# Performance work log

Measured on AMD Instinct MI355X. Metric: run time of the kernel, lower is better.

Reference implementation:

```python
import jax, jax.numpy as jnp
import numpy as np

N_NODES = 100000
D = 256          # embedding_dim
K = 5            # num_communities
B = 8192         # events in batch
R = 32           # negatives per event


def setup_inputs() -> dict:
    key = jax.random.key(0)
    ks = jax.random.split(key, 12)
    src = jax.random.randint(ks[0], (B,), 0, N_NODES)
    dst = jax.random.randint(ks[1], (B,), 0, N_NODES)
    neg = jax.random.randint(ks[2], (B, R), 0, N_NODES)
    ts = jax.random.uniform(ks[3], (B,), dtype=jnp.float32) * 100.0 + 50.0
    edge_idxs = jax.random.randint(ks[4], (B,), 0, 1000000)
    # node state table and last-update times (buffers in the torch module)
    state = jax.random.normal(ks[5], (N_NODES, D), dtype=jnp.float32)
    last_t = jax.random.uniform(ks[6], (N_NODES,), dtype=jnp.float32) * 50.0
    # decay parameter and CommunityProjector MLP params
    log_decay = jnp.asarray(0.0, dtype=jnp.float32)
    W1 = jax.random.normal(ks[7], (D, D), dtype=jnp.float32) / np.sqrt(D)
    b1 = jnp.zeros((D,), dtype=jnp.float32)
    W2 = jax.random.normal(ks[8], (D, K), dtype=jnp.float32) / np.sqrt(D)
    b2 = jnp.zeros((K,), dtype=jnp.float32)
    return {"src": src, "dst": dst, "neg": neg, "ts": ts, "edge_idxs": edge_idxs,
            "state": state, "last_t": last_t, "log_decay": log_decay,
            "W1": W1, "b1": b1, "W2": W2, "b2": b2}


def _proj_state(nodes, t, state, last_t, log_decay):
    # dt = clamp(t - last_t[nodes], 0); s_proj = state[nodes] * exp(-softplus(log_decay)*dt)
    dt = jnp.maximum(t - last_t[nodes], 0.0)
    decay = jax.nn.softplus(log_decay)
    gate = jnp.exp(-decay * dt)[..., None]
    return state[nodes] * gate


def _projector(x, W1, b1, W2, b2):
    # Linear -> ReLU -> (Dropout eval = identity) -> Linear -> Softmax
    h = jax.nn.relu(x @ W1 + b1)
    return jax.nn.softmax(h @ W2 + b2, axis=-1)


def reference(src, dst, neg, ts, edge_idxs, state, last_t, log_decay, W1, b1, W2, b2):
    s_src = _proj_state(src, ts, state, last_t, log_decay)          # [B, D]
    s_dst = _proj_state(dst, ts, state, last_t, log_decay)          # [B, D]
    s_neg = _proj_state(neg, ts[:, None], state, last_t, log_decay) # [B, R, D]
    p_src = _projector(s_src, W1, b1, W2, b2)                       # [B, K]
    p_dst = _projector(s_dst, W1, b1, W2, b2)                       # [B, K]
    p_neg = _projector(s_neg, W1, b1, W2, b2)                       # [B, R, K]
    return p_src, p_dst, p_neg
```

## Files before the change

### kernel.cpp

```cpp
#include <hip/hip_runtime.h>
#include <hip/hip_bf16.h>

#define B_EV    8192
#define R_NEG   32
#define DIM     256
#define K_COM   5
#define M_ROWS  (B_EV * (R_NEG + 2))
#define BM      64
#define NT      (M_ROWS / BM)
#define NBLK    512
#define N_NODES_C 100000

typedef _Float16 f16x8 __attribute__((ext_vector_type(8)));
typedef float    f32x4 __attribute__((ext_vector_type(4)));

__global__ __launch_bounds__(256, 2) void fused_kernel(
    const int* __restrict__ src, const int* __restrict__ dst,
    const int* __restrict__ neg, const float* __restrict__ ts,
    const float* __restrict__ state, const float* __restrict__ last_t,
    const float* __restrict__ log_decay,
    const float* __restrict__ W1, const float* __restrict__ b1,
    const float* __restrict__ W2, const float* __restrict__ b2,
    float* __restrict__ out)
{
    __shared__ f16x8 xt8[2048];
    __shared__ int   node_s[64];
    __shared__ float gate_s[64];
    __shared__ float part[4][64][K_COM];

    const int tid  = threadIdx.x;
    const int lane = tid & 63;
    const int w    = tid >> 6;
    const int l15  = lane & 15;
    const int g    = lane >> 4;

    float ld    = log_decay[0];
    float decay = (ld > 30.f) ? ld : log1pf(expf(ld));

    f16x8 bfrag[4][8];
    {
        const float* wbase = W1 + (size_t)(g * 8) * DIM + w * 64 + l15;
        #pragma unroll
        for (int nt = 0; nt < 4; ++nt)
            #pragma unroll
            for (int ks = 0; ks < 8; ++ks)
                #pragma unroll
                for (int j = 0; j < 8; ++j)
                    bfrag[nt][ks][j] = (_Float16)wbase[(size_t)(ks * 32 + j) * DIM + nt * 16];
    }

    for (int t = blockIdx.x; t < NT; t += NBLK) {
        const int m0 = t * BM;

        if (tid < 64) {
            int m  = m0 + tid;
            int be = m / 34;
            int sl = m - be * 34;
            int node = (sl == 0) ? src[be] : (sl == 1) ? dst[be] : neg[be * R_NEG + (sl - 2)];
            if ((unsigned)node >= (unsigned)N_NODES_C) node = 0;
            float dtv = fmaxf(ts[be] - last_t[node], 0.f);
            node_s[tid] = node;
            gate_s[tid] = expf(-decay * dtv);
        }
        __syncthreads();

        {
            int c8 = tid & 31;
            int rb = tid >> 5;
            #pragma unroll
            for (int it = 0; it < 8; ++it) {
                int r = it * 8 + rb;
                int node = node_s[r];
                float gg = gate_s[r];
                const float* sp = state + (size_t)node * DIM + c8 * 8;
                float4 v0 = *(const float4*)(sp);
                float4 v1 = *(const float4*)(sp + 4);
                f16x8 pk;
                pk[0] = (_Float16)(v0.x * gg); pk[1] = (_Float16)(v0.y * gg);
                pk[2] = (_Float16)(v0.z * gg); pk[3] = (_Float16)(v0.w * gg);
                pk[4] = (_Float16)(v1.x * gg); pk[5] = (_Float16)(v1.y * gg);
                pk[6] = (_Float16)(v1.z * gg); pk[7] = (_Float16)(v1.w * gg);
                xt8[(r * 32 + c8) ^ (r & 7)] = pk;
            }
        }
        __syncthreads();

        f32x4 acc[4][4];
        #pragma unroll
        for (int a = 0; a < 4; ++a)
            #pragma unroll
            for (int bb = 0; bb < 4; ++bb)
                acc[a][bb] = (f32x4){0.f, 0.f, 0.f, 0.f};

        #pragma unroll
        for (int ks = 0; ks < 8; ++ks) {
            f16x8 av[4];
            #pragma unroll
            for (int mt = 0; mt < 4; ++mt) {
                int row = mt * 16 + l15;
                av[mt] = xt8[(row * 32 + ks * 4 + g) ^ (row & 7)];
            }
            #pragma unroll
            for (int nt = 0; nt < 4; ++nt)
                #pragma unroll
                for (int mt = 0; mt < 4; ++mt)
                    acc[mt][nt] = __builtin_amdgcn_mfma_f32_16x16x32_f16(av[mt], bfrag[nt][ks], acc[mt][nt], 0, 0, 0);
        }

        float b1v[4];
        float w2v[4][K_COM];
        #pragma unroll
        for (int nt = 0; nt < 4; ++nt) {
            int col = w * 64 + nt * 16 + l15;
            b1v[nt] = b1[col];
            #pragma unroll
            for (int k = 0; k < K_COM; ++k) w2v[nt][k] = W2[col * K_COM + k];
        }

        #pragma unroll
        for (int mt = 0; mt < 4; ++mt) {
            #pragma unroll
            for (int reg = 0; reg < 4; ++reg) {
                float p[K_COM] = {0.f, 0.f, 0.f, 0.f, 0.f};
                #pragma unroll
                for (int nt = 0; nt < 4; ++nt) {
                    float h = fmaxf(acc[mt][nt][reg] + b1v[nt], 0.f);
                    #pragma unroll
                    for (int k = 0; k < K_COM; ++k) p[k] += h * w2v[nt][k];
                }
                #pragma unroll
                for (int off = 8; off >= 1; off >>= 1)
                    #pragma unroll
                    for (int k = 0; k < K_COM; ++k) p[k] += __shfl_xor(p[k], off);
                if (l15 == 0) {
                    int row = mt * 16 + g * 4 + reg;
                    #pragma unroll
                    for (int k = 0; k < K_COM; ++k) part[w][row][k] = p[k];
                }
            }
        }
        __syncthreads();

        if (tid < 64) {
            float lg[K_COM];
            #pragma unroll
            for (int k = 0; k < K_COM; ++k)
                lg[k] = part[0][tid][k] + part[1][tid][k] + part[2][tid][k] + part[3][tid][k] + b2[k];
            float mx = lg[0];
            #pragma unroll
            for (int k = 1; k < K_COM; ++k) mx = fmaxf(mx, lg[k]);
            float sum = 0.f;
            #pragma unroll
            for (int k = 0; k < K_COM; ++k) { lg[k] = expf(lg[k] - mx); sum += lg[k]; }
            float inv = 1.f / sum;

            int m  = m0 + tid;
            int be = m / 34;
            int sl = m - be * 34;
            float* op;
            if (sl == 0)      op = out + (size_t)be * K_COM;
            else if (sl == 1) op = out + (size_t)B_EV * K_COM + (size_t)be * K_COM;
            else              op = out + (size_t)2 * B_EV * K_COM + ((size_t)be * R_NEG + (sl - 2)) * K_COM;
            #pragma unroll
            for (int k = 0; k < K_COM; ++k) op[k] = lg[k] * inv;
        }
    }
}

extern "C" void kernel_launch(void* const* d_in, const int* in_sizes, int n_in,
                              void* d_out, int out_size, void* d_ws, size_t ws_size,
                              hipStream_t stream) {
    const int*   src       = (const int*)d_in[0];
    const int*   dst       = (const int*)d_in[1];
    const int*   neg       = (const int*)d_in[2];
    const float* ts        = (const float*)d_in[3];
    const float* state     = (const float*)d_in[5];
    const float* last_t    = (const float*)d_in[6];
    const float* log_decay = (const float*)d_in[7];
    const float* W1        = (const float*)d_in[8];
    const float* b1        = (const float*)d_in[9];
    const float* W2        = (const float*)d_in[10];
    const float* b2        = (const float*)d_in[11];

    fused_kernel<<<dim3(NBLK), dim3(256), 0, stream>>>(
        src, dst, neg, ts, state, last_t, log_decay, W1, b1, W2, b2,
        (float*)d_out);
}
```

Measured before the change: 326.0 us.

## Precompute state@W1 for all nodes, then gather and apply gate per row

The per-row decay gate is a scalar, so (state*gate)@W1 equals gate*(state@W1). The first kernel multiplies the whole 100k-node state table by W1 once and writes an fp16 table Y to the workspace. A second kernel gathers Y rows per event, applies the gate, bias, ReLU, the W2 projection and the softmax. This replaces a GEMM over about 278k gathered fp32 rows with a dense GEMM over 100k rows plus half-width gathers, at the cost of a 51 MB intermediate write and a second launch. The old fused kernel is kept as a fallback, with its W1 fragments unrolled into named registers, when the workspace is too small.

```diff
diff --git a/kernel.cpp b/kernel.cpp
--- a/kernel.cpp
+++ b/kernel.cpp
@@ -6,15 +6,216 @@
 #define DIM     256
 #define K_COM   5
 #define M_ROWS  (B_EV * (R_NEG + 2))
-#define BM      64
-#define NT      (M_ROWS / BM)
+#define NNODE   100000
+#define Y_BYTES ((size_t)NNODE * DIM * 2)
+#define S1_BLK  ((NNODE + 63) / 64)
+#define S2_BLK  2048
 #define NBLK    512
-#define N_NODES_C 100000
+#define NT_FB   (M_ROWS / 64)
 
 typedef _Float16 f16x8 __attribute__((ext_vector_type(8)));
 typedef float    f32x4 __attribute__((ext_vector_type(4)));
 
-__global__ __launch_bounds__(256, 2) void fused_kernel(
+#define MF(a, b, c) __builtin_amdgcn_mfma_f32_16x16x32_f16((a), (b), (c), 0, 0, 0)
+
+#define LDB2(BV, NT_, KS_) do {                                          \
+    const float* p_ = wbase + (size_t)((KS_) * 32) * DIM + (NT_) * 16;   \
+    BV[0] = (_Float16)p_[0 * DIM]; BV[1] = (_Float16)p_[1 * DIM];        \
+    BV[2] = (_Float16)p_[2 * DIM]; BV[3] = (_Float16)p_[3 * DIM];        \
+    BV[4] = (_Float16)p_[4 * DIM]; BV[5] = (_Float16)p_[5 * DIM];        \
+    BV[6] = (_Float16)p_[6 * DIM]; BV[7] = (_Float16)p_[7 * DIM];        \
+} while (0)
+
+#define KSTEP2(KS_, B0_, B1_) do {                                       \
+    f16x8 av0 = xt8[(( 0 + l15) * 32 + (KS_) * 4 + g) ^ (l15 & 7)];      \
+    f16x8 av1 = xt8[((16 + l15) * 32 + (KS_) * 4 + g) ^ (l15 & 7)];      \
+    f16x8 av2 = xt8[((32 + l15) * 32 + (KS_) * 4 + g) ^ (l15 & 7)];      \
+    f16x8 av3 = xt8[((48 + l15) * 32 + (KS_) * 4 + g) ^ (l15 & 7)];      \
+    acc[0][0] = MF(av0, B0_, acc[0][0]); acc[1][0] = MF(av1, B0_, acc[1][0]); \
+    acc[2][0] = MF(av2, B0_, acc[2][0]); acc[3][0] = MF(av3, B0_, acc[3][0]); \
+    acc[0][1] = MF(av0, B1_, acc[0][1]); acc[1][1] = MF(av1, B1_, acc[1][1]); \
+    acc[2][1] = MF(av2, B1_, acc[2][1]); acc[3][1] = MF(av3, B1_, acc[3][1]); \
+} while (0)
+
+__global__ __launch_bounds__(512, 2) void s1_gemm(
+    const float* __restrict__ state, const float* __restrict__ W1,
+    _Float16* __restrict__ Y)
+{
+    __shared__ f16x8 xt8[2048];
+    __shared__ f16x8 ot8[2048];
+
+    const int tid  = threadIdx.x;
+    const int lane = tid & 63;
+    const int w    = tid >> 6;
+    const int l15  = lane & 15;
+    const int g    = lane >> 4;
+    const int m0   = blockIdx.x * 64;
+
+    const float* wbase = W1 + (size_t)(g * 8) * DIM + w * 32 + l15;
+    f16x8 b00, b01, b02, b03, b04, b05, b06, b07;
+    f16x8 b10, b11, b12, b13, b14, b15, b16, b17;
+    LDB2(b00, 0, 0); LDB2(b01, 0, 1); LDB2(b02, 0, 2); LDB2(b03, 0, 3);
+    LDB2(b04, 0, 4); LDB2(b05, 0, 5); LDB2(b06, 0, 6); LDB2(b07, 0, 7);
+    LDB2(b10, 1, 0); LDB2(b11, 1, 1); LDB2(b12, 1, 2); LDB2(b13, 1, 3);
+    LDB2(b14, 1, 4); LDB2(b15, 1, 5); LDB2(b16, 1, 6); LDB2(b17, 1, 7);
+
+    #pragma unroll
+    for (int s = 0; s < 4; ++s) {
+        int cid = tid + s * 512;
+        int row = cid >> 5, c8 = cid & 31;
+        int m = m0 + row; if (m > NNODE - 1) m = NNODE - 1;
+        const float* sp = state + (size_t)m * DIM + c8 * 8;
+        float4 v0 = *(const float4*)(sp);
+        float4 v1 = *(const float4*)(sp + 4);
+        f16x8 pk;
+        pk[0] = (_Float16)v0.x; pk[1] = (_Float16)v0.y;
+        pk[2] = (_Float16)v0.z; pk[3] = (_Float16)v0.w;
+        pk[4] = (_Float16)v1.x; pk[5] = (_Float16)v1.y;
+        pk[6] = (_Float16)v1.z; pk[7] = (_Float16)v1.w;
+        xt8[row * 32 + (c8 ^ (row & 7))] = pk;
+    }
+    __syncthreads();
+
+    f32x4 acc[4][2];
+    #pragma unroll
+    for (int a = 0; a < 4; ++a) { acc[a][0] = (f32x4){0,0,0,0}; acc[a][1] = (f32x4){0,0,0,0}; }
+
+    KSTEP2(0, b00, b10); KSTEP2(1, b01, b11);
+    KSTEP2(2, b02, b12); KSTEP2(3, b03, b13);
+    KSTEP2(4, b04, b14); KSTEP2(5, b05, b15);
+    KSTEP2(6, b06, b16); KSTEP2(7, b07, b17);
+
+    _Float16* ot16 = (_Float16*)ot8;
+    #pragma unroll
+    for (int mt = 0; mt < 4; ++mt)
+        #pragma unroll
+        for (int nt = 0; nt < 2; ++nt) {
+            int c8o = w * 4 + nt * 2 + (l15 >> 3);
+            int j   = l15 & 7;
+            #pragma unroll
+            for (int reg = 0; reg < 4; ++reg) {
+                int row = mt * 16 + g * 4 + reg;
+                ot16[(row * 32 + (c8o ^ (row & 7))) * 8 + j] = (_Float16)acc[mt][nt][reg];
+            }
+        }
+    __syncthreads();
+
+    #pragma unroll
+    for (int s = 0; s < 4; ++s) {
+        int cid = tid + s * 512;
+        int row = cid >> 5, c8 = cid & 31;
+        int m = m0 + row;
+        if (m < NNODE)
+            *(f16x8*)(Y + (size_t)m * DIM + c8 * 8) = ot8[row * 32 + (c8 ^ (row & 7))];
+    }
+}
+
+__global__ void s2_head(
+    const int* __restrict__ src, const int* __restrict__ dst,
+    const int* __restrict__ neg, const float* __restrict__ ts,
+    const float* __restrict__ last_t, const float* __restrict__ log_decay,
+    const _Float16* __restrict__ Y, const float* __restrict__ b1,
+    const float* __restrict__ W2, const float* __restrict__ b2,
+    float* __restrict__ out)
+{
+    const int tid  = threadIdx.x;
+    const int lane = tid & 63;
+    const int grp  = lane >> 4;
+    const int l    = lane & 15;
+    const int wid  = blockIdx.x * 4 + (tid >> 6);
+
+    float ld    = log_decay[0];
+    float decay = (ld > 30.f) ? ld : log1pf(expf(ld));
+
+    float b1a[8], b1b[8], w2a[8][K_COM], w2b[8][K_COM];
+    #pragma unroll
+    for (int jj = 0; jj < 8; ++jj) {
+        int ca = l * 8 + jj, cb = 128 + l * 8 + jj;
+        b1a[jj] = b1[ca]; b1b[jj] = b1[cb];
+        #pragma unroll
+        for (int k = 0; k < K_COM; ++k) {
+            w2a[jj][k] = W2[ca * K_COM + k];
+            w2b[jj][k] = W2[cb * K_COM + k];
+        }
+    }
+    float bb[K_COM];
+    #pragma unroll
+    for (int k = 0; k < K_COM; ++k) bb[k] = b2[k];
+
+    for (int r4 = wid * 4; r4 < M_ROWS; r4 += S2_BLK * 4 * 4) {
+        int row = r4 + grp;
+        int be  = row / 34;
+        int sl  = row - be * 34;
+        int node = (sl == 0) ? src[be] : (sl == 1) ? dst[be] : neg[be * R_NEG + (sl - 2)];
+        if ((unsigned)node >= (unsigned)NNODE) node = 0;
+        float dtv  = fmaxf(ts[be] - last_t[node], 0.f);
+        float gate = expf(-decay * dtv);
+
+        const f16x8* yp = (const f16x8*)(Y + (size_t)node * DIM);
+        f16x8 y0 = yp[l];
+        f16x8 y1 = yp[16 + l];
+
+        float p[K_COM] = {0.f, 0.f, 0.f, 0.f, 0.f};
+        #pragma unroll
+        for (int jj = 0; jj < 8; ++jj) {
+            float h = fmaxf(fmaf(gate, (float)y0[jj], b1a[jj]), 0.f);
+            #pragma unroll
+            for (int k = 0; k < K_COM; ++k) p[k] = fmaf(h, w2a[jj][k], p[k]);
+            float h2 = fmaxf(fmaf(gate, (float)y1[jj], b1b[jj]), 0.f);
+            #pragma unroll
+            for (int k = 0; k < K_COM; ++k) p[k] = fmaf(h2, w2b[jj][k], p[k]);
+        }
+        #pragma unroll
+        for (int off = 8; off >= 1; off >>= 1)
+            #pragma unroll
+            for (int k = 0; k < K_COM; ++k) p[k] += __shfl_xor(p[k], off);
+
+        float lg[K_COM];
+        #pragma unroll
+        for (int k = 0; k < K_COM; ++k) lg[k] = p[k] + bb[k];
+        float mx = lg[0];
+        #pragma unroll
+        for (int k = 1; k < K_COM; ++k) mx = fmaxf(mx, lg[k]);
+        float sum = 0.f;
+        #pragma unroll
+        for (int k = 0; k < K_COM; ++k) { lg[k] = expf(lg[k] - mx); sum += lg[k]; }
+        float inv = 1.f / sum;
+
+        if (l == 0) {
+            float* op;
+            if (sl == 0)      op = out + (size_t)be * K_COM;
+            else if (sl == 1) op = out + (size_t)B_EV * K_COM + (size_t)be * K_COM;
+            else              op = out + (size_t)2 * B_EV * K_COM + ((size_t)be * R_NEG + (sl - 2)) * K_COM;
+            #pragma unroll
+            for (int k = 0; k < K_COM; ++k) op[k] = lg[k] * inv;
+        }
+    }
+}
+
+#define FLDB(BV, NT_, KS_) do {                                   \
+    const float* p_ = wbase + (size_t)((KS_) * 32) * DIM + (NT_) * 16; \
+    BV[0] = (_Float16)p_[0 * DIM]; BV[1] = (_Float16)p_[1 * DIM]; \
+    BV[2] = (_Float16)p_[2 * DIM]; BV[3] = (_Float16)p_[3 * DIM]; \
+    BV[4] = (_Float16)p_[4 * DIM]; BV[5] = (_Float16)p_[5 * DIM]; \
+    BV[6] = (_Float16)p_[6 * DIM]; BV[7] = (_Float16)p_[7 * DIM]; \
+} while (0)
+
+#define FKSTEP(KS_, B0_, B1_, B2_, B3_) do {                      \
+    f16x8 av0 = xt8[((0 * 16 + l15) * 32 + (KS_) * 4 + g) ^ (l15 & 7)]; \
+    f16x8 av1 = xt8[((1 * 16 + l15) * 32 + (KS_) * 4 + g) ^ (l15 & 7)]; \
+    f16x8 av2 = xt8[((2 * 16 + l15) * 32 + (KS_) * 4 + g) ^ (l15 & 7)]; \
+    f16x8 av3 = xt8[((3 * 16 + l15) * 32 + (KS_) * 4 + g) ^ (l15 & 7)]; \
+    acc[0][0] = MF(av0, B0_, acc[0][0]); acc[1][0] = MF(av1, B0_, acc[1][0]);  \
+    acc[2][0] = MF(av2, B0_, acc[2][0]); acc[3][0] = MF(av3, B0_, acc[3][0]);  \
+    acc[0][1] = MF(av0, B1_, acc[0][1]); acc[1][1] = MF(av1, B1_, acc[1][1]);  \
+    acc[2][1] = MF(av2, B1_, acc[2][1]); acc[3][1] = MF(av3, B1_, acc[3][1]);  \
+    acc[0][2] = MF(av0, B2_, acc[0][2]); acc[1][2] = MF(av1, B2_, acc[1][2]);  \
+    acc[2][2] = MF(av2, B2_, acc[2][2]); acc[3][2] = MF(av3, B2_, acc[3][2]);  \
+    acc[0][3] = MF(av0, B3_, acc[0][3]); acc[1][3] = MF(av1, B3_, acc[1][3]);  \
+    acc[2][3] = MF(av2, B3_, acc[2][3]); acc[3][3] = MF(av3, B3_, acc[3][3]);  \
+} while (0)
+
+__global__ __launch_bounds__(256, 2) void fused_fallback(
     const int* __restrict__ src, const int* __restrict__ dst,
     const int* __restrict__ neg, const float* __restrict__ ts,
     const float* __restrict__ state, const float* __restrict__ last_t,
@@ -37,33 +238,33 @@
     float ld    = log_decay[0];
     float decay = (ld > 30.f) ? ld : log1pf(expf(ld));
 
-    f16x8 bfrag[4][8];
-    {
-        const float* wbase = W1 + (size_t)(g * 8) * DIM + w * 64 + l15;
-        #pragma unroll
-        for (int nt = 0; nt < 4; ++nt)
-            #pragma unroll
-            for (int ks = 0; ks < 8; ++ks)
-                #pragma unroll
-                for (int j = 0; j < 8; ++j)
-                    bfrag[nt][ks][j] = (_Float16)wbase[(size_t)(ks * 32 + j) * DIM + nt * 16];
-    }
-
-    for (int t = blockIdx.x; t < NT; t += NBLK) {
-        const int m0 = t * BM;
-
+    const float* wbase = W1 + (size_t)(g * 8) * DIM + w * 64 + l15;
+    f16x8 b00, b01, b02, b03, b04, b05, b06, b07;
+    f16x8 b10, b11, b12, b13, b14, b15, b16, b17;
+    f16x8 b20, b21, b22, b23, b24, b25, b26, b27;
+    f16x8 b30, b31, b32, b33, b34, b35, b36, b37;
+    FLDB(b00, 0, 0); FLDB(b01, 0, 1); FLDB(b02, 0, 2); FLDB(b03, 0, 3);
+    FLDB(b04, 0, 4); FLDB(b05, 0, 5); FLDB(b06, 0, 6); FLDB(b07, 0, 7);
+    FLDB(b10, 1, 0); FLDB(b11, 1, 1); FLDB(b12, 1, 2); FLDB(b13, 1, 3);
+    FLDB(b14, 1, 4); FLDB(b15, 1, 5); FLDB(b16, 1, 6); FLDB(b17, 1, 7);
+    FLDB(b20, 2, 0); FLDB(b21, 2, 1); FLDB(b22, 2, 2); FLDB(b23, 2, 3);
+    FLDB(b24, 2, 4); FLDB(b25, 2, 5); FLDB(b26, 2, 6); FLDB(b27, 2, 7);
+    FLDB(b30, 3, 0); FLDB(b31, 3, 1); FLDB(b32, 3, 2); FLDB(b33, 3, 3);
+    FLDB(b34, 3, 4); FLDB(b35, 3, 5); FLDB(b36, 3, 6); FLDB(b37, 3, 7);
+
+    for (int t = blockIdx.x; t < NT_FB; t += NBLK) {
+        const int m0 = t * 64;
         if (tid < 64) {
             int m  = m0 + tid;
             int be = m / 34;
             int sl = m - be * 34;
             int node = (sl == 0) ? src[be] : (sl == 1) ? dst[be] : neg[be * R_NEG + (sl - 2)];
-            if ((unsigned)node >= (unsigned)N_NODES_C) node = 0;
+            if ((unsigned)node >= (unsigned)NNODE) node = 0;
             float dtv = fmaxf(ts[be] - last_t[node], 0.f);
             node_s[tid] = node;
             gate_s[tid] = expf(-decay * dtv);
         }
         __syncthreads();
-
         {
             int c8 = tid & 31;
             int rb = tid >> 5;
@@ -89,23 +290,12 @@
         #pragma unroll
         for (int a = 0; a < 4; ++a)
             #pragma unroll
-            for (int bb = 0; bb < 4; ++bb)
-                acc[a][bb] = (f32x4){0.f, 0.f, 0.f, 0.f};
-
-        #pragma unroll
-        for (int ks = 0; ks < 8; ++ks) {
-            f16x8 av[4];
-            #pragma unroll
-            for (int mt = 0; mt < 4; ++mt) {
-                int row = mt * 16 + l15;
-                av[mt] = xt8[(row * 32 + ks * 4 + g) ^ (row & 7)];
-            }
-            #pragma unroll
-            for (int nt = 0; nt < 4; ++nt)
-                #pragma unroll
-                for (int mt = 0; mt < 4; ++mt)
-                    acc[mt][nt] = __builtin_amdgcn_mfma_f32_16x16x32_f16(av[mt], bfrag[nt][ks], acc[mt][nt], 0, 0, 0);
-        }
+            for (int bq = 0; bq < 4; ++bq) acc[a][bq] = (f32x4){0,0,0,0};
+
+        FKSTEP(0, b00, b10, b20, b30); FKSTEP(1, b01, b11, b21, b31);
+        FKSTEP(2, b02, b12, b22, b32); FKSTEP(3, b03, b13, b23, b33);
+        FKSTEP(4, b04, b14, b24, b34); FKSTEP(5, b05, b15, b25, b35);
+        FKSTEP(6, b06, b16, b26, b36); FKSTEP(7, b07, b17, b27, b37);
 
         float b1v[4];
         float w2v[4][K_COM];
@@ -116,9 +306,8 @@
             #pragma unroll
             for (int k = 0; k < K_COM; ++k) w2v[nt][k] = W2[col * K_COM + k];
         }
-
-        #pragma unroll
-        for (int mt = 0; mt < 4; ++mt) {
+        #pragma unroll
+        for (int mt = 0; mt < 4; ++mt)
             #pragma unroll
             for (int reg = 0; reg < 4; ++reg) {
                 float p[K_COM] = {0.f, 0.f, 0.f, 0.f, 0.f};
@@ -138,7 +327,6 @@
                     for (int k = 0; k < K_COM; ++k) part[w][row][k] = p[k];
                 }
             }
-        }
         __syncthreads();
 
         if (tid < 64) {
@@ -153,7 +341,6 @@
             #pragma unroll
             for (int k = 0; k < K_COM; ++k) { lg[k] = expf(lg[k] - mx); sum += lg[k]; }
             float inv = 1.f / sum;
-
             int m  = m0 + tid;
             int be = m / 34;
             int sl = m - be * 34;
@@ -182,7 +369,14 @@
     const float* W2        = (const float*)d_in[10];
     const float* b2        = (const float*)d_in[11];
 
-    fused_kernel<<<dim3(NBLK), dim3(256), 0, stream>>>(
-        src, dst, neg, ts, state, last_t, log_decay, W1, b1, W2, b2,
-        (float*)d_out);
+    if (ws_size >= Y_BYTES) {
+        _Float16* Y = (_Float16*)d_ws;
+        s1_gemm<<<dim3(S1_BLK), dim3(512), 0, stream>>>(state, W1, Y);
+        s2_head<<<dim3(S2_BLK), dim3(256), 0, stream>>>(
+            src, dst, neg, ts, last_t, log_decay, Y, b1, W2, b2, (float*)d_out);
+    } else {
+        fused_fallback<<<dim3(NBLK), dim3(256), 0, stream>>>(
+            src, dst, neg, ts, state, last_t, log_decay, W1, b1, W2, b2,
+            (float*)d_out);
+    }
 }
```

Result: faster. 282.6 us (-13.3%).
